# Kernel optimization log

Measured on AMD Instinct MI355X. Metric: run time of the kernel, lower is better.

The kernel has to match this reference:

```python
import jax, jax.numpy as jnp
import numpy as np

jax.config.update("jax_enable_x64", True)

STEPS = 50
WIN = 8
NUM_GRAPHS = 100
ORDER = 500           # nodes per graph
DEG = 16              # out-degree of every node
N = NUM_GRAPHS * ORDER
NUM_INTS = (ORDER + 62) // 63  # int64 words per node in adj_bits (63-bit packing)


def setup_inputs() -> dict:
    rng = np.random.default_rng(0)
    node_local = np.arange(N, dtype=np.int64) % ORDER          # per-graph local id
    graph_base = (np.arange(N, dtype=np.int64) // ORDER) * ORDER
    # sample DEG neighbors per node within its own graph, no self loops
    r = rng.integers(0, ORDER - 1, size=(N, DEG), dtype=np.int64)
    nb_local = (node_local[:, None] + 1 + r) % ORDER            # (N, DEG) local ids
    adj_nodes = (graph_base[:, None] + nb_local).reshape(-1).astype(np.int64)
    degrees = np.full(N, DEG, dtype=np.int64)
    adj_offset = (np.arange(N, dtype=np.int64) * DEG)
    # bit-packed adjacency: bit (local_id % 63) of word (local_id // 63)
    adj_bits = np.zeros((N, NUM_INTS), dtype=np.int64)
    rows = np.repeat(np.arange(N), DEG)
    cols = (nb_local // 63).reshape(-1)
    vals = (np.int64(1) << (nb_local % 63)).reshape(-1)
    np.bitwise_or.at(adj_bits, (rows, cols), vals)
    choices = rng.integers(0, 2 ** 62, size=(STEPS, N), dtype=np.int64)
    x = rng.standard_normal((N, 16)).astype(np.float32)
    return {
        "adj_nodes": jnp.asarray(adj_nodes),
        "adj_offset": jnp.asarray(adj_offset),
        "degrees": jnp.asarray(degrees),
        "node_id": jnp.asarray(node_local),
        "adj_bits": jnp.asarray(adj_bits),
        "choices": jnp.asarray(choices),
        "x": jnp.asarray(x),
    }


def reference(adj_nodes, adj_offset, degrees, node_id, adj_bits, choices, x):
    s = WIN
    n = degrees.shape[0]
    start = jnp.arange(n, dtype=jnp.int64)  # eval path; all degrees > 0 by construction
    w = n
    nb_degrees = jnp.where(degrees == 1, degrees, degrees - 1)

    window0 = jnp.zeros((s, w), jnp.int64).at[-1].set(start)  # window[j] = walks[i+1-s+j]
    valid0 = jnp.zeros((s,), bool).at[-1].set(True)

    def step(carry, ch):
        window, valid = carry
        cur = window[-1]
        deg = degrees[cur]
        off = adj_offset[cur]
        edge_idx = ch % deg
        chosen = off + edge_idx
        new = adj_nodes[chosen]
        # non-backtracking correction (walk_mode != 'uniform'); no-op at step 0
        bt = (new == window[-2]) & valid[-2]
        alt = off + (edge_idx + 1 + ch % nb_degrees[cur]) % deg
        chosen = jnp.where(bt, alt, chosen)
        new = jnp.where(bt, adj_nodes[alt], new)
        vmask = valid[:, None]                     # (s,1)
        id_row = (new[None, :] == window) & vmask  # (s,w) identity encoding
        cur_id = node_id[new]
        safe_win = jnp.where(vmask, window, 0)
        bits = adj_bits[safe_win, (cur_id // 63)[None, :]]           # (s,w)
        edge_row = (((bits >> (cur_id % 63)[None, :]) % 2) == 1) & vmask
        window = jnp.concatenate([window[1:], new[None, :]], axis=0)
        valid = jnp.concatenate([valid[1:], jnp.ones((1,), bool)], axis=0)
        return (window, valid), (new, chosen, id_row, edge_row)

    (_, _), (nodes_seq, edges_seq, id_rows, edge_rows) = jax.lax.scan(
        step, (window0, valid0), choices)

    walks = jnp.concatenate([start[None, :], nodes_seq], axis=0)              # (l, w)
    id_enc = jnp.concatenate([jnp.zeros((1, s, w), bool), id_rows], axis=0)   # (l, s, w)
    adj_enc = jnp.concatenate([jnp.zeros((1, s, w), bool), edge_rows], axis=0)

    walk_nodes = walks.T                 # (w, l)
    walk_edges = edges_seq.T             # (w, l-1)
    id_feat = id_enc.transpose(2, 1, 0).astype(jnp.float32)          # (w, s, l)
    adj_feat = adj_enc.transpose(2, 1, 0).astype(jnp.float32)[:, :-1, :]  # (w, s-1, l)
    walk_x = jnp.concatenate([id_feat, adj_feat], axis=1)            # (w, 2s-1, l)
    return walk_nodes, walk_edges, walk_x
```

## Files before the change

### kernel.cpp

```cpp
#include <hip/hip_runtime.h>
#include <stdint.h>

#define WIN 8
#define DEG 16
#define ORDER 500
#define STEPS_C 50
#define T1 51
#define FRD 15
#define NI 8
#define WPB 125
#define BLOCK 256
#define MSTR 17
#define NSTR 52

__global__ __launch_bounds__(256)
void fused_kernel(const int* __restrict__ adj_nodes,
                  const int* __restrict__ adj_bits,
                  const int* __restrict__ choices,
                  float* __restrict__ out, int N)
{
    __shared__ unsigned long long smem[6440];
    unsigned short* g_adj  = (unsigned short*)smem;
    int*            g_bits = (int*)((char*)smem + 16000);
    unsigned long long* mask_l = smem;
    unsigned short* nodes_l = (unsigned short*)((char*)smem + 32000);
    unsigned char*  eidx_l  = (unsigned char*)((char*)smem + 45000);

    const int tid = threadIdx.x;

    const int nwg = gridDim.x;
    const int q8  = nwg >> 3;
    const int vb  = ((nwg & 7) == 0) ? ((blockIdx.x & 7) * q8 + (blockIdx.x >> 3))
                                     : blockIdx.x;

    const int graph  = vb >> 2;
    const int lb     = vb & 3;
    const int gbase  = graph * ORDER;
    const int lstart = lb * WPB + tid;
    const bool act   = (tid < WPB);
    const int wi     = gbase + lstart;
    const int wild   = act ? wi : gbase;
    const int wbase  = vb * WPB;

    {
        const int4* src = (const int4*)(adj_nodes + (size_t)gbase * DEG);
        unsigned* dst = (unsigned*)g_adj;
        for (int c = tid; c < ORDER * DEG / 4; c += BLOCK) {
            const int4 v = src[c];
            dst[2 * c + 0] = (unsigned)(v.x - gbase) | ((unsigned)(v.y - gbase) << 16);
            dst[2 * c + 1] = (unsigned)(v.z - gbase) | ((unsigned)(v.w - gbase) << 16);
        }
        int4* db = (int4*)g_bits;
        const int4* sb = (const int4*)(adj_bits + (size_t)gbase * NI);
        for (int c = tid; c < ORDER * NI / 4; c += BLOCK) db[c] = sb[c];
    }
    __syncthreads();

    unsigned long long idm[WIN];
    unsigned long long adm[WIN - 1];
#pragma unroll
    for (int k = 0; k < WIN; k++) idm[k] = 0ull;
#pragma unroll
    for (int k = 0; k < WIN - 1; k++) adm[k] = 0ull;

    if (act) {
        int w[WIN];
#pragma unroll
        for (int k = 0; k < WIN; k++) w[k] = 0;
        w[7] = lstart;

        nodes_l[tid * NSTR] = (unsigned short)lstart;

        int c0 = choices[wild];
        int c1 = choices[(size_t)1 * N + wild];
        int c2 = choices[(size_t)2 * N + wild];
        int c3 = choices[(size_t)3 * N + wild];
        int c4 = choices[(size_t)4 * N + wild];
        int c5 = choices[(size_t)5 * N + wild];
        int c6 = choices[(size_t)6 * N + wild];
        int c7 = choices[(size_t)7 * N + wild];

        for (int t = 0; t < STEPS_C; t++) {
            const int ch = c0;
            c0 = c1; c1 = c2; c2 = c3; c3 = c4; c4 = c5; c5 = c6; c6 = c7;
            c7 = (t + 8 < STEPS_C) ? choices[(size_t)(t + 8) * N + wild] : 0;

            const int e = ch & (DEG - 1);
            int r15 = ch % (DEG - 1); if (r15 < 0) r15 += (DEG - 1);
            const int e2 = (e + 1 + r15) & (DEG - 1);

            const int cur = w[7];
            const int n1 = g_adj[cur * DEG + e];
            const int n2 = g_adj[cur * DEG + e2];

            const bool bt = (t >= 1) && (n1 == w[6]);
            const int nn = bt ? n2 : n1;
            const int ee = bt ? e2 : e;

            const unsigned q  = (unsigned)nn / 63u;
            const unsigned rr = (unsigned)nn - q * 63u;
            const unsigned s  = rr > 31u ? 31u : rr;
            const unsigned long long bitpos = 1ull << (t + 1);

#pragma unroll
            for (int k = 0; k < WIN; k++) {
                const bool vk = (k + t) >= (WIN - 1);
                if (vk && (w[k] == nn)) idm[k] |= bitpos;
            }
#pragma unroll
            for (int k = 0; k < WIN - 1; k++) {
                const bool vk = (k + t) >= (WIN - 1);
                const int word = g_bits[w[k] * NI + q];
                if (vk && ((word >> s) & 1)) adm[k] |= bitpos;
            }

#pragma unroll
            for (int k = 0; k < WIN - 1; k++) w[k] = w[k + 1];
            w[7] = nn;

            nodes_l[tid * NSTR + t + 1] = (unsigned short)nn;
            eidx_l[tid * NSTR + t]      = (unsigned char)ee;
        }
    }

    __syncthreads();
    if (act) {
#pragma unroll
        for (int k = 0; k < WIN; k++)      mask_l[tid * MSTR + k]     = idm[k];
#pragma unroll
        for (int k = 0; k < WIN - 1; k++)  mask_l[tid * MSTR + 8 + k] = adm[k];
    }
    __syncthreads();


    {
        float* dst = out + (size_t)wbase * T1;
        const int count = WPB * T1;
        const int head = (4 - (int)((((uintptr_t)dst) >> 2) & 3)) & 3;
        for (int i = tid; i < head; i += BLOCK) {
            const int wl = i / T1, t = i - wl * T1;
            dst[i] = (float)(gbase + (int)nodes_l[wl * NSTR + t]);
        }
        const int n4 = (count - head) >> 2;
        for (int c = tid; c < n4; c += BLOCK) {
            const int f0 = head + (c << 2);
            int wl = f0 / T1, t = f0 - wl * T1;
            float vv[4];
#pragma unroll
            for (int u = 0; u < 4; u++) {
                vv[u] = (float)(gbase + (int)nodes_l[wl * NSTR + t]);
                t++; if (t == T1) { t = 0; wl++; }
            }
            float4 v; v.x = vv[0]; v.y = vv[1]; v.z = vv[2]; v.w = vv[3];
            *reinterpret_cast<float4*>(dst + f0) = v;
        }
        const int done = head + (n4 << 2);
        for (int i = done + tid; i < count; i += BLOCK) {
            const int wl = i / T1, t = i - wl * T1;
            dst[i] = (float)(gbase + (int)nodes_l[wl * NSTR + t]);
        }
    }

    {
        float* dst = out + (size_t)N * T1 + (size_t)wbase * STEPS_C;
        const int count = WPB * STEPS_C;
        const int head = (4 - (int)((((uintptr_t)dst) >> 2) & 3)) & 3;
        for (int i = tid; i < head; i += BLOCK) {
            const int wl = i / STEPS_C, t = i - wl * STEPS_C;
            dst[i] = (float)((((gbase + (int)nodes_l[wl * NSTR + t])) << 4)
                             + (int)eidx_l[wl * NSTR + t]);
        }
        const int n4 = (count - head) >> 2;
        for (int c = tid; c < n4; c += BLOCK) {
            const int f0 = head + (c << 2);
            int wl = f0 / STEPS_C, t = f0 - wl * STEPS_C;
            float vv[4];
#pragma unroll
            for (int u = 0; u < 4; u++) {
                vv[u] = (float)((((gbase + (int)nodes_l[wl * NSTR + t])) << 4)
                                + (int)eidx_l[wl * NSTR + t]);
                t++; if (t == STEPS_C) { t = 0; wl++; }
            }
            float4 v; v.x = vv[0]; v.y = vv[1]; v.z = vv[2]; v.w = vv[3];
            *reinterpret_cast<float4*>(dst + f0) = v;
        }
        const int done = head + (n4 << 2);
        for (int i = done + tid; i < count; i += BLOCK) {
            const int wl = i / STEPS_C, t = i - wl * STEPS_C;
            dst[i] = (float)((((gbase + (int)nodes_l[wl * NSTR + t])) << 4)
                             + (int)eidx_l[wl * NSTR + t]);
        }
    }

    {
        float* dst = out + (size_t)N * (T1 + STEPS_C) + (size_t)wbase * (FRD * T1);
        const int count = WPB * FRD * T1;
        const int head = (4 - (int)((((uintptr_t)dst) >> 2) & 3)) & 3;
        for (int i = tid; i < head; i += BLOCK) {
            const int wl = i / (FRD * T1), rem = i - wl * (FRD * T1);
            const int j = rem / T1, t = rem - j * T1;
            dst[i] = ((mask_l[wl * MSTR + j] >> t) & 1ull) ? 1.0f : 0.0f;
        }
        const int n4 = (count - head) >> 2;
        for (int c = tid; c < n4; c += BLOCK) {
            const int f0 = head + (c << 2);
            int wl = f0 / (FRD * T1), rem = f0 - wl * (FRD * T1);
            int j = rem / T1, t = rem - j * T1;
            float vv[4];
#pragma unroll
            for (int u = 0; u < 4; u++) {
                vv[u] = ((mask_l[wl * MSTR + j] >> t) & 1ull) ? 1.0f : 0.0f;
                t++;
                if (t == T1) { t = 0; j++; if (j == FRD) { j = 0; wl++; } }
            }
            float4 v; v.x = vv[0]; v.y = vv[1]; v.z = vv[2]; v.w = vv[3];
            *reinterpret_cast<float4*>(dst + f0) = v;
        }
        const int done = head + (n4 << 2);
        for (int i = done + tid; i < count; i += BLOCK) {
            const int wl = i / (FRD * T1), rem = i - wl * (FRD * T1);
            const int j = rem / T1, t = rem - j * T1;
            dst[i] = ((mask_l[wl * MSTR + j] >> t) & 1ull) ? 1.0f : 0.0f;
        }
    }
}

extern "C" void kernel_launch(void* const* d_in, const int* in_sizes, int n_in,
                              void* d_out, int out_size, void* d_ws, size_t ws_size,
                              hipStream_t stream) {
    const int N = in_sizes[3];
    const int num_graphs = N / ORDER;
    const int grid = num_graphs * 4;

    fused_kernel<<<grid, BLOCK, 0, stream>>>(
        (const int*)d_in[0], (const int*)d_in[4], (const int*)d_in[5],
        (float*)d_out, N);
}
```

Before: 60.56 us.

## Compute identity and adjacency features in parallel during output write

Drops the per-walk serial computation of identity and adjacency bitmasks from the walk loop, which tracked a window of past nodes and did seven shared-memory bit lookups per step. Each feature value is now computed on the fly in the final store loop by comparing stored node ids and reading the adjacency bits, spread over all 256 threads. This shortens the serial walk, frees the mask registers and removes one barrier. In exchange the output phase does more shared-memory reads and more arithmetic per element.

Result: slower. 99.55 us (+64.4%).

```diff
diff --git a/kernel.cpp b/kernel.cpp
--- a/kernel.cpp
+++ b/kernel.cpp
@@ -10,7 +10,6 @@
 #define NI 8
 #define WPB 125
 #define BLOCK 256
-#define MSTR 17
 #define NSTR 52
 
 __global__ __launch_bounds__(256)
@@ -20,9 +19,8 @@
                   float* __restrict__ out, int N)
 {
     __shared__ unsigned long long smem[6440];
-    unsigned short* g_adj  = (unsigned short*)smem;
-    int*            g_bits = (int*)((char*)smem + 16000);
-    unsigned long long* mask_l = smem;
+    unsigned short* g_adj   = (unsigned short*)smem;
+    int*            g_bits  = (int*)((char*)smem + 16000);
     unsigned short* nodes_l = (unsigned short*)((char*)smem + 32000);
     unsigned char*  eidx_l  = (unsigned char*)((char*)smem + 45000);
 
@@ -56,18 +54,9 @@
     }
     __syncthreads();
 
-    unsigned long long idm[WIN];
-    unsigned long long adm[WIN - 1];
-#pragma unroll
-    for (int k = 0; k < WIN; k++) idm[k] = 0ull;
-#pragma unroll
-    for (int k = 0; k < WIN - 1; k++) adm[k] = 0ull;
-
     if (act) {
-        int w[WIN];
-#pragma unroll
-        for (int k = 0; k < WIN; k++) w[k] = 0;
-        w[7] = lstart;
+        int prev = -1;
+        int cur  = lstart;
 
         nodes_l[tid * NSTR] = (unsigned short)lstart;
 
@@ -89,46 +78,19 @@
             int r15 = ch % (DEG - 1); if (r15 < 0) r15 += (DEG - 1);
             const int e2 = (e + 1 + r15) & (DEG - 1);
 
-            const int cur = w[7];
             const int n1 = g_adj[cur * DEG + e];
             const int n2 = g_adj[cur * DEG + e2];
 
-            const bool bt = (t >= 1) && (n1 == w[6]);
+            const bool bt = (t >= 1) && (n1 == prev);
             const int nn = bt ? n2 : n1;
             const int ee = bt ? e2 : e;
 
-            const unsigned q  = (unsigned)nn / 63u;
-            const unsigned rr = (unsigned)nn - q * 63u;
-            const unsigned s  = rr > 31u ? 31u : rr;
-            const unsigned long long bitpos = 1ull << (t + 1);
-
-#pragma unroll
-            for (int k = 0; k < WIN; k++) {
-                const bool vk = (k + t) >= (WIN - 1);
-                if (vk && (w[k] == nn)) idm[k] |= bitpos;
-            }
-#pragma unroll
-            for (int k = 0; k < WIN - 1; k++) {
-                const bool vk = (k + t) >= (WIN - 1);
-                const int word = g_bits[w[k] * NI + q];
-                if (vk && ((word >> s) & 1)) adm[k] |= bitpos;
-            }
-
-#pragma unroll
-            for (int k = 0; k < WIN - 1; k++) w[k] = w[k + 1];
-            w[7] = nn;
-
             nodes_l[tid * NSTR + t + 1] = (unsigned short)nn;
             eidx_l[tid * NSTR + t]      = (unsigned char)ee;
-        }
-    }
-
-    __syncthreads();
-    if (act) {
-#pragma unroll
-        for (int k = 0; k < WIN; k++)      mask_l[tid * MSTR + k]     = idm[k];
-#pragma unroll
-        for (int k = 0; k < WIN - 1; k++)  mask_l[tid * MSTR + 8 + k] = adm[k];
+
+            prev = cur;
+            cur  = nn;
+        }
     }
     __syncthreads();
 
@@ -196,10 +158,28 @@
         float* dst = out + (size_t)N * (T1 + STEPS_C) + (size_t)wbase * (FRD * T1);
         const int count = WPB * FRD * T1;
         const int head = (4 - (int)((((uintptr_t)dst) >> 2) & 3)) & 3;
+
+        auto feat = [&](int wl, int j, int t) -> float {
+            const int base = wl * NSTR;
+            if (j < 8) {
+                const int src = t - 8 + j;
+                return (src >= 0 && nodes_l[base + t] == nodes_l[base + src])
+                       ? 1.0f : 0.0f;
+            } else {
+                const int src = t - 16 + j;
+                if (src < 0) return 0.0f;
+                const int a = (int)nodes_l[base + src];
+                const int b = (int)nodes_l[base + t];
+                const unsigned q  = (unsigned)b / 63u;
+                const unsigned rr = (unsigned)b - q * 63u;
+                const unsigned s  = rr > 31u ? 31u : rr;
+                return ((g_bits[a * NI + q] >> s) & 1) ? 1.0f : 0.0f;
+            }
+        };
+
         for (int i = tid; i < head; i += BLOCK) {
             const int wl = i / (FRD * T1), rem = i - wl * (FRD * T1);
-            const int j = rem / T1, t = rem - j * T1;
-            dst[i] = ((mask_l[wl * MSTR + j] >> t) & 1ull) ? 1.0f : 0.0f;
+            dst[i] = feat(wl, rem / T1, rem % T1);
         }
         const int n4 = (count - head) >> 2;
         for (int c = tid; c < n4; c += BLOCK) {
@@ -209,7 +189,7 @@
             float vv[4];
 #pragma unroll
             for (int u = 0; u < 4; u++) {
-                vv[u] = ((mask_l[wl * MSTR + j] >> t) & 1ull) ? 1.0f : 0.0f;
+                vv[u] = feat(wl, j, t);
                 t++;
                 if (t == T1) { t = 0; j++; if (j == FRD) { j = 0; wl++; } }
             }
@@ -219,8 +199,7 @@
         const int done = head + (n4 << 2);
         for (int i = done + tid; i < count; i += BLOCK) {
             const int wl = i / (FRD * T1), rem = i - wl * (FRD * T1);
-            const int j = rem / T1, t = rem - j * T1;
-            dst[i] = ((mask_l[wl * MSTR + j] >> t) & 1ull) ? 1.0f : 0.0f;
+            dst[i] = feat(wl, rem / T1, rem % T1);
         }
     }
 }
```
